# Kernel optimization log

Measured on AMD Instinct MI355X. Metric: run time of the kernel, lower is better.

The kernel has to match this reference:

```python
import jax, jax.numpy as jnp
import numpy as np

N = 8192          # num nodes
E = 262144        # num edges
F_IN = 512        # dataset.num_features
HID = 256         # hidden_dim
C = 16            # dataset.num_classes
ALPHA = 1.0
GAMMA = 1.0
EPS = 0.4
LN_EPS = 1e-5


def setup_inputs() -> dict:
    key = jax.random.key(0)
    ks = jax.random.split(key, 16)
    x = jax.random.normal(ks[0], (N, F_IN), dtype=jnp.float32)
    edge_index = jax.random.randint(ks[1], (2, E), 0, N, dtype=jnp.int64)
    def lin(k, fan_in, fan_out):
        s = 1.0 / np.sqrt(fan_in)
        return jax.random.uniform(k, (fan_in, fan_out), jnp.float32, -s, s)
    return {
        "x": x,
        "edge_index": edge_index,
        "W0": lin(ks[2], F_IN, HID), "b0": jnp.zeros((HID,), jnp.float32),
        "ln0_g": jnp.ones((HID,), jnp.float32), "ln0_b": jnp.zeros((HID,), jnp.float32),
        "W1": lin(ks[3], HID, HID), "b1": jnp.zeros((HID,), jnp.float32),
        "ln1_g": jnp.ones((HID,), jnp.float32), "ln1_b": jnp.zeros((HID,), jnp.float32),
        "W2": lin(ks[4], HID, C), "b2": jnp.zeros((C,), jnp.float32),
    }


def _layernorm(h, g, b):
    mu = jnp.mean(h, axis=-1, keepdims=True)
    var = jnp.var(h, axis=-1, keepdims=True)
    return (h - mu) * jax.lax.rsqrt(var + LN_EPS) * g + b


def _hpf_weight_matrix(edge_index, n, dtype):
    # to_dense_adj with parallel-edge accumulation
    A = jnp.zeros((n, n), dtype).at[edge_index[0], edge_index[1]].add(jnp.asarray(1.0, dtype))
    eye = jnp.eye(n, dtype=dtype)
    A = GAMMA * A + ALPHA * eye
    # D^{-1/2} A D^{-1/2} as fused row/col scaling (same math as the two diag matmuls)
    dinv = jax.lax.rsqrt(jnp.sum(A, axis=1))
    A_hat = dinv[:, None] * A * dinv[None, :]
    # (eps - 1) I + (I - A_hat) == eps*I - A_hat ; keep only positive entries (edge extraction)
    U = EPS * eye - A_hat
    return jnp.where(U > 0, U, jnp.asarray(0.0, dtype))


def reference(x, edge_index, W0, b0, ln0_g, ln0_b, W1, b1, ln1_g, ln1_b, W2, b2):
    Wmat = _hpf_weight_matrix(edge_index, x.shape[0], x.dtype)
    # GCNConv(normalize=False): h' = scatter_{src->tgt}(w * (h@W)[src]) + bias == Wmat^T @ (h@W) + b
    def gcn(h, W, b):
        return Wmat.T @ (h @ W) + b
    h = gcn(x, W0, b0)
    h = _layernorm(jax.nn.relu(h), ln0_g, ln0_b)   # dropout p=0.0 -> identity
    h = gcn(h, W1, b1)
    h = _layernorm(jax.nn.relu(h), ln1_g, ln1_b)
    embedding = gcn(h, W2, b2)
    return embedding, jax.nn.log_softmax(embedding, axis=1)
```

## Files before the change

### kernel.cpp

```cpp
#include <hip/hip_runtime.h>

#define NN 8192
#define NE 262144
#define FIN 512
#define HIDN 256
#define NC 16

typedef __attribute__((ext_vector_type(8))) short bf16x8;
typedef __attribute__((ext_vector_type(4))) short bf16x4;
typedef __attribute__((ext_vector_type(4))) float f32x4;

static __device__ __forceinline__ unsigned short f2bf(float f) {
    union { float f; unsigned u; } v; v.f = f;
    unsigned r = v.u + 0x7FFFu + ((v.u >> 16) & 1u);
    return (unsigned short)(r >> 16);
}

__global__ __launch_bounds__(256) void deg_kernel(const int* __restrict__ ei,
                                                  int* __restrict__ cnt) {
    int e0 = (blockIdx.x * 256 + threadIdx.x) * 4;
    int4 s = *(const int4*)&ei[e0];
    int4 t = *(const int4*)&ei[NE + e0];
    atomicAdd(&cnt[s.x], 1);
    atomicAdd(&cnt[s.y], 1);
    atomicAdd(&cnt[s.z], 1);
    atomicAdd(&cnt[s.w], 1);
    if (s.x == t.x) atomicAdd(&cnt[NN + s.x], 1);
    if (s.y == t.y) atomicAdd(&cnt[NN + s.y], 1);
    if (s.z == t.z) atomicAdd(&cnt[NN + s.z], 1);
    if (s.w == t.w) atomicAdd(&cnt[NN + s.w], 1);
}

template<int K, int N>
static __device__ __forceinline__ void pack_w(const float* __restrict__ W,
                                              unsigned short* __restrict__ Wp, int f) {
    constexpr int KC = K / 32;
    int lane = f & 63;
    int g = f >> 6;
    int kc = g % KC;
    int nt = g / KC;
    int n = nt * 16 + (lane & 15);
    int kbase = kc * 32 + (lane >> 4) * 8;
    bf16x8 v;
#pragma unroll
    for (int j = 0; j < 8; ++j) v[j] = (short)f2bf(W[(kbase + j) * N + n]);
    *(bf16x8*)&Wp[f * 8] = v;
}

__global__ __launch_bounds__(256) void prep_kernel(const int* __restrict__ cnt,
                                                   const float* __restrict__ W0,
                                                   const float* __restrict__ W1,
                                                   const float* __restrict__ W2,
                                                   float* __restrict__ wd,
                                                   unsigned short* __restrict__ Wp0,
                                                   unsigned short* __restrict__ Wp1,
                                                   unsigned short* __restrict__ Wp2) {
    int b = blockIdx.x, tid = threadIdx.x;
    if (b < 64) {
        pack_w<512, 256>(W0, Wp0, b * 256 + tid);
    } else if (b < 96) {
        pack_w<256, 256>(W1, Wp1, (b - 64) * 256 + tid);
    } else if (b < 98) {
        pack_w<256, 16>(W2, Wp2, (b - 96) * 256 + tid);
    } else {
        int i = (b - 98) * 256 + tid;
        float deg = 1.0f + (float)cnt[i];
        float sl  = 1.0f + (float)cnt[NN + i];
        float u = 0.4f - sl / deg;
        wd[i] = u > 0.0f ? u : 0.0f;
    }
}

static __device__ __forceinline__ void ln_epilogue(
    const f32x4 acc[4], const float* __restrict__ bias, const float* __restrict__ gam,
    const float* __restrict__ bet, const float wdr[4],
    int half, int wq, int quad, int l16,
    unsigned short* sH, float red[][8])
{
    float bv[4], gv[4], btv[4];
#pragma unroll
    for (int nt = 0; nt < 4; ++nt) {
        int col = wq * 64 + nt * 16 + l16;
        bv[nt] = bias[col]; gv[nt] = gam[col]; btv[nt] = bet[col];
    }
    float vv[4][4], s[4], ss[4];
#pragma unroll
    for (int reg = 0; reg < 4; ++reg) {
        float ps = 0.f, pss = 0.f;
#pragma unroll
        for (int nt = 0; nt < 4; ++nt) {
            float v = fmaxf(fmaf(wdr[reg], acc[nt][reg], bv[nt]), 0.f);
            vv[nt][reg] = v;
            ps += v; pss += v * v;
        }
        s[reg] = ps; ss[reg] = pss;
    }
#pragma unroll
    for (int off = 1; off < 16; off <<= 1)
#pragma unroll
        for (int reg = 0; reg < 4; ++reg) {
            s[reg]  += __shfl_xor(s[reg],  off, 64);
            ss[reg] += __shfl_xor(ss[reg], off, 64);
        }
    __syncthreads();
    if (l16 == 0) {
#pragma unroll
        for (int reg = 0; reg < 4; ++reg) {
            int rl = half * 16 + quad * 4 + reg;
            red[rl][wq * 2]     = s[reg];
            red[rl][wq * 2 + 1] = ss[reg];
        }
    }
    __syncthreads();
#pragma unroll
    for (int reg = 0; reg < 4; ++reg) {
        int rl = half * 16 + quad * 4 + reg;
        float ts  = red[rl][0] + red[rl][2] + red[rl][4] + red[rl][6];
        float tss = red[rl][1] + red[rl][3] + red[rl][5] + red[rl][7];
        float mu  = ts * (1.0f / 256.0f);
        float var = tss * (1.0f / 256.0f) - mu * mu;
        float rs  = rsqrtf(var + 1e-5f);
#pragma unroll
        for (int nt = 0; nt < 4; ++nt) {
            float o = (vv[nt][reg] - mu) * rs * gv[nt] + btv[nt];
            sH[rl * 264 + wq * 64 + nt * 16 + l16] = f2bf(o);
        }
    }
    __syncthreads();
}

__global__ __launch_bounds__(512) void mega_kernel(
    const float* __restrict__ x,
    const unsigned short* __restrict__ Wp0, const unsigned short* __restrict__ Wp1,
    const unsigned short* __restrict__ Wp2,
    const float* __restrict__ b0, const float* __restrict__ g0, const float* __restrict__ be0,
    const float* __restrict__ b1, const float* __restrict__ g1, const float* __restrict__ be1,
    const float* __restrict__ b2, const float* __restrict__ wd,
    float* __restrict__ out)
{
    __shared__ unsigned short sX[32 * 136];
    __shared__ unsigned short sH[32 * 264];
    __shared__ float red[32][8];

    const int tid  = threadIdx.x;
    const int lane = tid & 63, wave = tid >> 6;
    const int quad = lane >> 4, l16 = lane & 15;
    const int half = wave >> 2, wq = wave & 3;
    const int row0 = blockIdx.x * 32;

    float wdr[4];
#pragma unroll
    for (int reg = 0; reg < 4; ++reg) wdr[reg] = wd[row0 + half * 16 + quad * 4 + reg];

    const bf16x8* Wp0v = (const bf16x8*)Wp0;
    const bf16x8* Wp1v = (const bf16x8*)Wp1;
    const bf16x8* Wp2v = (const bf16x8*)Wp2;
    const float4* x4 = (const float4*)x;

    f32x4 acc[4];
#pragma unroll
    for (int nt = 0; nt < 4; ++nt) acc[nt] = (f32x4){0.f, 0.f, 0.f, 0.f};

    for (int kb = 0; kb < 4; ++kb) {
#pragma unroll
        for (int i = 0; i < 2; ++i) {
            int f = tid + i * 512;
            int r = f >> 5, c4 = f & 31;
            float4 v = x4[(row0 + r) * 128 + kb * 32 + c4];
            bf16x4 h;
            h[0] = (short)f2bf(v.x); h[1] = (short)f2bf(v.y);
            h[2] = (short)f2bf(v.z); h[3] = (short)f2bf(v.w);
            *(bf16x4*)&sX[r * 136 + c4 * 4] = h;
        }
        __syncthreads();
#pragma unroll
        for (int kc = 0; kc < 4; ++kc) {
            bf16x8 a = *(const bf16x8*)&sX[(half * 16 + l16) * 136 + kc * 32 + quad * 8];
#pragma unroll
            for (int nt = 0; nt < 4; ++nt) {
                bf16x8 b = Wp0v[((wq * 4 + nt) * 16 + kb * 4 + kc) * 64 + lane];
                acc[nt] = __builtin_amdgcn_mfma_f32_16x16x32_bf16(a, b, acc[nt], 0, 0, 0);
            }
        }
        __syncthreads();
    }
    ln_epilogue(acc, b0, g0, be0, wdr, half, wq, quad, l16, sH, red);

    f32x4 acc1[4];
#pragma unroll
    for (int nt = 0; nt < 4; ++nt) acc1[nt] = (f32x4){0.f, 0.f, 0.f, 0.f};
#pragma unroll
    for (int kc = 0; kc < 8; ++kc) {
        bf16x8 a = *(const bf16x8*)&sH[(half * 16 + l16) * 264 + kc * 32 + quad * 8];
#pragma unroll
        for (int nt = 0; nt < 4; ++nt) {
            bf16x8 b = Wp1v[((wq * 4 + nt) * 8 + kc) * 64 + lane];
            acc1[nt] = __builtin_amdgcn_mfma_f32_16x16x32_bf16(a, b, acc1[nt], 0, 0, 0);
        }
    }
    ln_epilogue(acc1, b1, g1, be1, wdr, half, wq, quad, l16, sH, red);

    if (wq == 0) {
        f32x4 acch = (f32x4){0.f, 0.f, 0.f, 0.f};
#pragma unroll
        for (int kc = 0; kc < 8; ++kc) {
            bf16x8 a = *(const bf16x8*)&sH[(half * 16 + l16) * 264 + kc * 32 + quad * 8];
            bf16x8 b = Wp2v[kc * 64 + lane];
            acch = __builtin_amdgcn_mfma_f32_16x16x32_bf16(a, b, acch, 0, 0, 0);
        }
        float bb = b2[l16];
#pragma unroll
        for (int reg = 0; reg < 4; ++reg) {
            int row = row0 + half * 16 + quad * 4 + reg;
            float v = fmaf(wdr[reg], acch[reg], bb);
            float m = v;
#pragma unroll
            for (int off = 8; off >= 1; off >>= 1) m = fmaxf(m, __shfl_xor(m, off, 64));
            float e = __expf(v - m);
            float se = e;
#pragma unroll
            for (int off = 8; off >= 1; off >>= 1) se += __shfl_xor(se, off, 64);
            float lsm = (v - m) - __logf(se);
            out[row * 16 + l16] = v;
            out[NN * 16 + row * 16 + l16] = lsm;
        }
    }
}

extern "C" void kernel_launch(void* const* d_in, const int* in_sizes, int n_in,
                              void* d_out, int out_size, void* d_ws, size_t ws_size,
                              hipStream_t stream) {
    const float* x  = (const float*)d_in[0];
    const int*   ei = (const int*)d_in[1];
    const float* W0 = (const float*)d_in[2];
    const float* b0 = (const float*)d_in[3];
    const float* g0 = (const float*)d_in[4];
    const float* be0 = (const float*)d_in[5];
    const float* W1 = (const float*)d_in[6];
    const float* b1 = (const float*)d_in[7];
    const float* g1 = (const float*)d_in[8];
    const float* be1 = (const float*)d_in[9];
    const float* W2 = (const float*)d_in[10];
    const float* b2 = (const float*)d_in[11];
    float* out = (float*)d_out;

    char* ws = (char*)d_ws;
    int*            cnt = (int*)ws;
    float*          wd  = (float*)(ws + 64 * 1024);
    unsigned short* Wp0 = (unsigned short*)(ws + 96 * 1024);
    unsigned short* Wp1 = (unsigned short*)(ws + 352 * 1024);
    unsigned short* Wp2 = (unsigned short*)(ws + 480 * 1024);

    hipMemsetAsync(cnt, 0, 2 * NN * sizeof(int), stream);
    deg_kernel<<<NE / 1024, 256, 0, stream>>>(ei, cnt);
    prep_kernel<<<130, 256, 0, stream>>>(cnt, W0, W1, W2, wd, Wp0, Wp1, Wp2);
    mega_kernel<<<NN / 32, 512, 0, stream>>>(x, Wp0, Wp1, Wp2,
                                             b0, g0, be0, b1, g1, be1, b2, wd, out);
}
```

Measured before the change: 112.9 us.

## Fuse memset, degree, weight packing and main kernel into one cooperative launch

```diff
diff --git a/kernel.cpp b/kernel.cpp
--- a/kernel.cpp
+++ b/kernel.cpp
@@ -1,4 +1,7 @@
 #include <hip/hip_runtime.h>
+#include <hip/hip_cooperative_groups.h>
+
+namespace cg = cooperative_groups;
 
 #define NN 8192
 #define NE 262144
@@ -14,21 +17,6 @@
     union { float f; unsigned u; } v; v.f = f;
     unsigned r = v.u + 0x7FFFu + ((v.u >> 16) & 1u);
     return (unsigned short)(r >> 16);
-}
-
-__global__ __launch_bounds__(256) void deg_kernel(const int* __restrict__ ei,
-                                                  int* __restrict__ cnt) {
-    int e0 = (blockIdx.x * 256 + threadIdx.x) * 4;
-    int4 s = *(const int4*)&ei[e0];
-    int4 t = *(const int4*)&ei[NE + e0];
-    atomicAdd(&cnt[s.x], 1);
-    atomicAdd(&cnt[s.y], 1);
-    atomicAdd(&cnt[s.z], 1);
-    atomicAdd(&cnt[s.w], 1);
-    if (s.x == t.x) atomicAdd(&cnt[NN + s.x], 1);
-    if (s.y == t.y) atomicAdd(&cnt[NN + s.y], 1);
-    if (s.z == t.z) atomicAdd(&cnt[NN + s.z], 1);
-    if (s.w == t.w) atomicAdd(&cnt[NN + s.w], 1);
 }
 
 template<int K, int N>
@@ -47,30 +35,6 @@
     *(bf16x8*)&Wp[f * 8] = v;
 }
 
-__global__ __launch_bounds__(256) void prep_kernel(const int* __restrict__ cnt,
-                                                   const float* __restrict__ W0,
-                                                   const float* __restrict__ W1,
-                                                   const float* __restrict__ W2,
-                                                   float* __restrict__ wd,
-                                                   unsigned short* __restrict__ Wp0,
-                                                   unsigned short* __restrict__ Wp1,
-                                                   unsigned short* __restrict__ Wp2) {
-    int b = blockIdx.x, tid = threadIdx.x;
-    if (b < 64) {
-        pack_w<512, 256>(W0, Wp0, b * 256 + tid);
-    } else if (b < 96) {
-        pack_w<256, 256>(W1, Wp1, (b - 64) * 256 + tid);
-    } else if (b < 98) {
-        pack_w<256, 16>(W2, Wp2, (b - 96) * 256 + tid);
-    } else {
-        int i = (b - 98) * 256 + tid;
-        float deg = 1.0f + (float)cnt[i];
-        float sl  = 1.0f + (float)cnt[NN + i];
-        float u = 0.4f - sl / deg;
-        wd[i] = u > 0.0f ? u : 0.0f;
-    }
-}
-
 static __device__ __forceinline__ void ln_epilogue(
     const f32x4 acc[4], const float* __restrict__ bias, const float* __restrict__ gam,
     const float* __restrict__ bet, const float wdr[4],
@@ -129,28 +93,60 @@
     __syncthreads();
 }
 
-__global__ __launch_bounds__(512) void mega_kernel(
-    const float* __restrict__ x,
-    const unsigned short* __restrict__ Wp0, const unsigned short* __restrict__ Wp1,
-    const unsigned short* __restrict__ Wp2,
+__global__ __launch_bounds__(512) void fused_kernel(
+    const float* __restrict__ x, const int* __restrict__ ei,
+    const float* __restrict__ W0, const float* __restrict__ W1, const float* __restrict__ W2,
     const float* __restrict__ b0, const float* __restrict__ g0, const float* __restrict__ be0,
     const float* __restrict__ b1, const float* __restrict__ g1, const float* __restrict__ be1,
-    const float* __restrict__ b2, const float* __restrict__ wd,
+    const float* __restrict__ b2,
+    int* __restrict__ cnt,
+    unsigned short* __restrict__ Wp0, unsigned short* __restrict__ Wp1,
+    unsigned short* __restrict__ Wp2,
     float* __restrict__ out)
 {
     __shared__ unsigned short sX[32 * 136];
     __shared__ unsigned short sH[32 * 264];
     __shared__ float red[32][8];
+    __shared__ float swd[32];
 
     const int tid  = threadIdx.x;
+    const int bid  = blockIdx.x;
+    const int gt   = bid * 512 + tid;
     const int lane = tid & 63, wave = tid >> 6;
     const int quad = lane >> 4, l16 = lane & 15;
     const int half = wave >> 2, wq = wave & 3;
-    const int row0 = blockIdx.x * 32;
-
+    const int row0 = bid * 32;
+
+    if (gt < 2 * NN)
+        __hip_atomic_store(&cnt[gt], 0, __ATOMIC_RELAXED, __HIP_MEMORY_SCOPE_AGENT);
+    int gp = (255 - bid) * 512 + tid;
+    if (gp < 16384)       pack_w<512, 256>(W0, Wp0, gp);
+    else if (gp < 24576)  pack_w<256, 256>(W1, Wp1, gp - 16384);
+    else if (gp < 25088)  pack_w<256, 16 >(W2, Wp2, gp - 24576);
+
+    cg::this_grid().sync();
+
+    {
+        int2 s2 = *(const int2*)&ei[gt * 2];
+        int2 t2 = *(const int2*)&ei[NE + gt * 2];
+        atomicAdd(&cnt[s2.x], 1);
+        atomicAdd(&cnt[s2.y], 1);
+        if (s2.x == t2.x) atomicAdd(&cnt[NN + s2.x], 1);
+        if (s2.y == t2.y) atomicAdd(&cnt[NN + s2.y], 1);
+    }
+
+    cg::this_grid().sync();
+
+    if (tid < 32) {
+        int d  = __hip_atomic_load(&cnt[row0 + tid],      __ATOMIC_RELAXED, __HIP_MEMORY_SCOPE_AGENT);
+        int sl = __hip_atomic_load(&cnt[NN + row0 + tid], __ATOMIC_RELAXED, __HIP_MEMORY_SCOPE_AGENT);
+        float u = 0.4f - (1.0f + (float)sl) / (1.0f + (float)d);
+        swd[tid] = u > 0.0f ? u : 0.0f;
+    }
+    __syncthreads();
     float wdr[4];
 #pragma unroll
-    for (int reg = 0; reg < 4; ++reg) wdr[reg] = wd[row0 + half * 16 + quad * 4 + reg];
+    for (int reg = 0; reg < 4; ++reg) wdr[reg] = swd[half * 16 + quad * 4 + reg];
 
     const bf16x8* Wp0v = (const bf16x8*)Wp0;
     const bf16x8* Wp1v = (const bf16x8*)Wp1;
@@ -246,14 +242,13 @@
 
     char* ws = (char*)d_ws;
     int*            cnt = (int*)ws;
-    float*          wd  = (float*)(ws + 64 * 1024);
-    unsigned short* Wp0 = (unsigned short*)(ws + 96 * 1024);
-    unsigned short* Wp1 = (unsigned short*)(ws + 352 * 1024);
-    unsigned short* Wp2 = (unsigned short*)(ws + 480 * 1024);
-
-    hipMemsetAsync(cnt, 0, 2 * NN * sizeof(int), stream);
-    deg_kernel<<<NE / 1024, 256, 0, stream>>>(ei, cnt);
-    prep_kernel<<<130, 256, 0, stream>>>(cnt, W0, W1, W2, wd, Wp0, Wp1, Wp2);
-    mega_kernel<<<NN / 32, 512, 0, stream>>>(x, Wp0, Wp1, Wp2,
-                                             b0, g0, be0, b1, g1, be1, b2, wd, out);
-}
+    unsigned short* Wp0 = (unsigned short*)(ws + 64 * 1024);
+    unsigned short* Wp1 = (unsigned short*)(ws + 320 * 1024);
+    unsigned short* Wp2 = (unsigned short*)(ws + 448 * 1024);
+
+    void* args[] = { &x, &ei, &W0, &W1, &W2,
+                     &b0, &g0, &be0, &b1, &g1, &be1, &b2,
+                     &cnt, &Wp0, &Wp1, &Wp2, &out };
+    hipLaunchCooperativeKernel((const void*)fused_kernel, dim3(NN / 32), dim3(512),
+                               args, 0, stream);
+}
```

Measured after the change: 180.8 us. +60.1%, slower.
